# Kernel tuning notes

Measured on AMD Instinct MI355X. Metric: run time of the kernel, lower is better.

The kernel has to match this reference:

```python
import jax, jax.numpy as jnp
import numpy as np

N_NODES = 100000
N_EDGES = 1600000
IN_C = 128
HID = 128
OUT_C = 16
BN_EPS = 1e-5


def _uniform(key, shape, fan_in):
    lim = 1.0 / np.sqrt(fan_in)
    return jax.random.uniform(key, shape, jnp.float32, -lim, lim)


def setup_inputs() -> dict:
    key = jax.random.key(0)
    ks = jax.random.split(key, 24)
    inp = {
        "x": jax.random.normal(ks[0], (N_NODES, IN_C), jnp.float32),
        "edge_index": jax.random.randint(ks[1], (2, N_EDGES), 0, N_NODES, dtype=jnp.int32),
    }
    dims = [(IN_C, HID), (HID, HID), (HID, OUT_C)]
    for l, (fi, fo) in enumerate(dims):
        inp[f"Wn{l}"] = _uniform(ks[2 + 3 * l], (fi, fo), fi)   # lin_l (neighbor) weight
        inp[f"b{l}"] = _uniform(ks[3 + 3 * l], (fo,), fi)        # lin_l bias
        inp[f"Ws{l}"] = _uniform(ks[4 + 3 * l], (fi, fo), fi)   # lin_r (self/root) weight, no bias
    for l in range(2):  # BatchNorm params for the first num_layers-1 layers (eval mode)
        inp[f"g{l}"] = jnp.ones((HID,), jnp.float32)
        inp[f"be{l}"] = jnp.zeros((HID,), jnp.float32)
        inp[f"rm{l}"] = jax.random.normal(ks[12 + 2 * l], (HID,), jnp.float32) * 0.1
        inp[f"rv{l}"] = jax.random.uniform(ks[13 + 2 * l], (HID,), jnp.float32, 0.5, 1.5)
    return inp


def _sage_conv(h, src, dst, Wn, b, Ws):
    # PyG SAGEConv (aggr='mean'): out = lin_l(mean_{j in N(i)} x_j) + lin_r(x_i)
    n = h.shape[0]
    msg = h[src]                                                   # [E, F] gather
    s = jax.ops.segment_sum(msg, dst, num_segments=n)              # [N, F]
    cnt = jax.ops.segment_sum(jnp.ones((src.shape[0], 1), h.dtype), dst, num_segments=n)
    agg = s / jnp.maximum(cnt, 1.0)                                # mean over neighbors
    return agg @ Wn + b + h @ Ws


def _bn_eval(h, g, be, rm, rv):
    return (h - rm) * jax.lax.rsqrt(rv + BN_EPS) * g + be


def reference(x, edge_index, Wn0, b0, Ws0, Wn1, b1, Ws1, Wn2, b2, Ws2,
              g0, be0, rm0, rv0, g1, be1, rm1, rv1):
    src, dst = edge_index[0], edge_index[1]
    h = _sage_conv(x, src, dst, Wn0, b0, Ws0)
    h = jax.nn.relu(_bn_eval(h, g0, be0, rm0, rv0))   # eval: dropout is identity
    h = _sage_conv(h, src, dst, Wn1, b1, Ws1)
    h = jax.nn.relu(_bn_eval(h, g1, be1, rm1, rv1))
    return _sage_conv(h, src, dst, Wn2, b2, Ws2)
```

## Files before the change

kernel.cpp:

```cpp
#include <hip/hip_runtime.h>
#include <hip/hip_bf16.h>


constexpr int N   = 100000;
constexpr int E   = 1600000;
constexpr int F   = 128;
constexpr int FO  = 16;
constexpr int CAP = 64;

typedef __attribute__((ext_vector_type(8))) short bf16x8;
typedef __attribute__((ext_vector_type(4))) float f32x4;

__device__ __forceinline__ ushort f2bf(float v) {
  return __bfloat16_as_ushort(__float2bfloat16(v));
}
__device__ __forceinline__ float bf2f(ushort u) {
  return __uint_as_float(((unsigned)u) << 16);
}
__device__ __forceinline__ float bf_lo(unsigned u) {
  return __uint_as_float(u << 16);
}
__device__ __forceinline__ float bf_hi(unsigned u) {
  return __uint_as_float(u & 0xffff0000u);
}

__global__ void fill_k(const int* __restrict__ src, const int* __restrict__ dst,
                       int* __restrict__ degc, int* __restrict__ slots) {
  int i = blockIdx.x * blockDim.x + threadIdx.x;
  int stride = gridDim.x * blockDim.x;
  for (; i < E; i += stride) {
    int d = dst[i];
    int pos = atomicAdd(&degc[d], 1);
    if (pos < CAP) slots[(size_t)d * CAP + pos] = src[i];
  }
}

__global__ void pack_bt_k(const float* __restrict__ Wn, const float* __restrict__ Ws,
                          ushort* __restrict__ Bt) {
  int t = blockIdx.x * blockDim.x + threadIdx.x;
  int n = t >> 7;
  int k = t & 127;
  float w = (n < 128) ? Wn[k * F + n] : Ws[k * F + (n - 128)];
  Bt[t] = f2bf(w);
}

__global__ __launch_bounds__(256) void dual_gemm_mfma_k(
    const float* __restrict__ h_in, const ushort* __restrict__ Bt,
    const float* __restrict__ b,
    ushort* __restrict__ y, float* __restrict__ s) {
  __shared__ uint4 AsU[2048];
  char* Ahi = reinterpret_cast<char*>(AsU);
  char* Alo = Ahi + 64 * 256;
  const int tid = threadIdx.x;
  const int row0 = blockIdx.x * 64;

#pragma unroll
  for (int j = 0; j < 4; ++j) {
    int f = tid + j * 256;
    int row = f >> 4;
    int kc = f & 15;
    int gr = row0 + row; if (gr >= N) gr = N - 1;
    const float4* gp = reinterpret_cast<const float4*>(h_in + (size_t)gr * F + kc * 8);
    float4 v0 = gp[0], v1 = gp[1];
    float vv[8] = {v0.x, v0.y, v0.z, v0.w, v1.x, v1.y, v1.z, v1.w};
    unsigned ph[4], pl[4];
#pragma unroll
    for (int q = 0; q < 4; ++q) {
      ushort h0 = f2bf(vv[2 * q]);
      ushort h1 = f2bf(vv[2 * q + 1]);
      ushort l0 = f2bf(vv[2 * q] - bf2f(h0));
      ushort l1 = f2bf(vv[2 * q + 1] - bf2f(h1));
      ph[q] = (unsigned)h0 | ((unsigned)h1 << 16);
      pl[q] = (unsigned)l0 | ((unsigned)l1 << 16);
    }
    int off = (row * 256 + kc * 16) ^ ((row & 7) << 4);
    *reinterpret_cast<uint4*>(Ahi + off) = make_uint4(ph[0], ph[1], ph[2], ph[3]);
    *reinterpret_cast<uint4*>(Alo + off) = make_uint4(pl[0], pl[1], pl[2], pl[3]);
  }
  __syncthreads();

  const int lane = tid & 63;
  const int wave = tid >> 6;
  const int wcol0 = wave * 64;
  const int lg = lane >> 4;
  const int lr = lane & 15;

  f32x4 acc[4][4];
#pragma unroll
  for (int r = 0; r < 4; ++r)
#pragma unroll
    for (int c = 0; c < 4; ++c) acc[r][c] = f32x4{0.f, 0.f, 0.f, 0.f};

#pragma unroll
  for (int kk = 0; kk < 4; ++kk) {
    bf16x8 bfr[4];
#pragma unroll
    for (int c = 0; c < 4; ++c) {
      int col = wcol0 + c * 16 + lr;
      bfr[c] = *reinterpret_cast<const bf16x8*>(Bt + (size_t)col * F + kk * 32 + lg * 8);
    }
#pragma unroll
    for (int r = 0; r < 4; ++r) {
      int row = r * 16 + lr;
      int off = (row * 256 + kk * 64 + lg * 16) ^ ((row & 7) << 4);
      bf16x8 a = *reinterpret_cast<const bf16x8*>(Ahi + off);
#pragma unroll
      for (int c = 0; c < 4; ++c)
        acc[r][c] = __builtin_amdgcn_mfma_f32_16x16x32_bf16(a, bfr[c], acc[r][c], 0, 0, 0);
    }
#pragma unroll
    for (int r = 0; r < 4; ++r) {
      int row = r * 16 + lr;
      int off = (row * 256 + kk * 64 + lg * 16) ^ ((row & 7) << 4);
      bf16x8 a = *reinterpret_cast<const bf16x8*>(Alo + off);
#pragma unroll
      for (int c = 0; c < 4; ++c)
        acc[r][c] = __builtin_amdgcn_mfma_f32_16x16x32_bf16(a, bfr[c], acc[r][c], 0, 0, 0);
    }
  }

  if (wave < 2) {
#pragma unroll
    for (int r = 0; r < 4; ++r)
#pragma unroll
      for (int c = 0; c < 4; ++c) {
        int col = wcol0 + c * 16 + lr;
#pragma unroll
        for (int q = 0; q < 4; ++q) {
          int grow = row0 + r * 16 + lg * 4 + q;
          if (grow < N) y[(size_t)grow * F + col] = f2bf(acc[r][c][q]);
        }
      }
  } else {
#pragma unroll
    for (int r = 0; r < 4; ++r)
#pragma unroll
      for (int c = 0; c < 4; ++c) {
        int scol = wcol0 - 128 + c * 16 + lr;
        float bias = b[scol];
#pragma unroll
        for (int q = 0; q < 4; ++q) {
          int grow = row0 + r * 16 + lg * 4 + q;
          if (grow < N) s[(size_t)grow * F + scol] = acc[r][c][q] + bias;
        }
      }
  }
}

__global__ __launch_bounds__(256) void agg_epi_k(
    const int* __restrict__ degc, const int* __restrict__ slots,
    const ushort* __restrict__ y, const float* __restrict__ s,
    const float* __restrict__ g, const float* __restrict__ be,
    const float* __restrict__ rm, const float* __restrict__ rv,
    float* __restrict__ h_out) {
  const int node = blockIdx.x * 4 + (threadIdx.x >> 6);
  const int c2 = threadIdx.x & 63;
  int deg = degc[node]; if (deg > CAP) deg = CAP;
  const int* sl = slots + (size_t)node * CAP;

  float a0 = 0.f, a1 = 0.f, a2 = 0.f, a3 = 0.f;
  float b0 = 0.f, b1 = 0.f, b2 = 0.f, b3 = 0.f;
  int e = 0;
  for (; e + 4 <= deg; e += 4) {
    int n0 = sl[e], n1 = sl[e + 1], n2 = sl[e + 2], n3 = sl[e + 3];
    unsigned u0 = *reinterpret_cast<const unsigned*>(y + (size_t)n0 * F + c2 * 2);
    unsigned u1 = *reinterpret_cast<const unsigned*>(y + (size_t)n1 * F + c2 * 2);
    unsigned u2 = *reinterpret_cast<const unsigned*>(y + (size_t)n2 * F + c2 * 2);
    unsigned u3 = *reinterpret_cast<const unsigned*>(y + (size_t)n3 * F + c2 * 2);
    a0 += bf_lo(u0); b0 += bf_hi(u0);
    a1 += bf_lo(u1); b1 += bf_hi(u1);
    a2 += bf_lo(u2); b2 += bf_hi(u2);
    a3 += bf_lo(u3); b3 += bf_hi(u3);
  }
  for (; e < deg; ++e) {
    unsigned u = *reinterpret_cast<const unsigned*>(y + (size_t)sl[e] * F + c2 * 2);
    a0 += bf_lo(u); b0 += bf_hi(u);
  }
  const float inv = 1.0f / fmaxf((float)deg, 1.0f);
  const float mlo = ((a0 + a1) + (a2 + a3)) * inv;
  const float mhi = ((b0 + b1) + (b2 + b3)) * inv;

  const int cA = 2 * c2;
  float2 sv = *reinterpret_cast<const float2*>(s + (size_t)node * F + cA);
  float2 gv = *reinterpret_cast<const float2*>(g + cA);
  float2 bev = *reinterpret_cast<const float2*>(be + cA);
  float2 rmv = *reinterpret_cast<const float2*>(rm + cA);
  float2 rvv = *reinterpret_cast<const float2*>(rv + cA);
  float olo = (mlo + sv.x - rmv.x) * (rsqrtf(rvv.x + 1e-5f) * gv.x) + bev.x;
  float ohi = (mhi + sv.y - rmv.y) * (rsqrtf(rvv.y + 1e-5f) * gv.y) + bev.y;
  float2 o = make_float2(fmaxf(olo, 0.f), fmaxf(ohi, 0.f));
  *reinterpret_cast<float2*>(h_out + (size_t)node * F + cA) = o;
}

__global__ __launch_bounds__(256) void gemm2_k(
    const float* __restrict__ h_in,
    const float* __restrict__ Wn, const float* __restrict__ Ws,
    const float* __restrict__ b,
    ushort* __restrict__ y2, float* __restrict__ s2) {
  __shared__ float hL[16][F];
  const int tid = threadIdx.x;
  const int row0 = blockIdx.x * 16;
#pragma unroll
  for (int j = 0; j < 2; ++j) {
    int f = tid + j * 256;
    int r = f >> 5;
    int cc = f & 31;
    reinterpret_cast<float4*>(&hL[r][0])[cc] =
        reinterpret_cast<const float4*>(h_in + (size_t)(row0 + r) * F)[cc];
  }
  __syncthreads();

  const int c = tid & 15;
  const int r = tid >> 4;
  float ay = 0.f, as = 0.f;
  for (int k0 = 0; k0 < F; k0 += 4) {
    float4 hv = *reinterpret_cast<const float4*>(&hL[r][k0]);
    ay += hv.x * Wn[(k0 + 0) * FO + c] + hv.y * Wn[(k0 + 1) * FO + c]
        + hv.z * Wn[(k0 + 2) * FO + c] + hv.w * Wn[(k0 + 3) * FO + c];
    as += hv.x * Ws[(k0 + 0) * FO + c] + hv.y * Ws[(k0 + 1) * FO + c]
        + hv.z * Ws[(k0 + 2) * FO + c] + hv.w * Ws[(k0 + 3) * FO + c];
  }
  y2[(size_t)(row0 + r) * FO + c] = f2bf(ay);
  s2[(size_t)(row0 + r) * FO + c] = as + b[c];
}

__global__ __launch_bounds__(256) void agg_out_k(
    const int* __restrict__ degc, const int* __restrict__ slots,
    const ushort* __restrict__ y2, const float* __restrict__ s2,
    float* __restrict__ out) {
  const int node = blockIdx.x * 4 + (threadIdx.x >> 6);
  const int lane = threadIdx.x & 63;
  const int c = lane & 15;
  const int j = lane >> 4;
  int deg = degc[node]; if (deg > CAP) deg = CAP;
  const int* sl = slots + (size_t)node * CAP;
  float acc = 0.f;
  for (int e = j; e < deg; e += 4) {
    unsigned bits = y2[(size_t)sl[e] * FO + c];
    acc += __uint_as_float(bits << 16);
  }
  acc += __shfl_xor(acc, 16, 64);
  acc += __shfl_xor(acc, 32, 64);
  if (j == 0)
    out[(size_t)node * FO + c] = acc / fmaxf((float)deg, 1.0f) + s2[(size_t)node * FO + c];
}

extern "C" void kernel_launch(void* const* d_in, const int* in_sizes, int n_in,
                              void* d_out, int out_size, void* d_ws, size_t ws_size,
                              hipStream_t stream) {
  const float* x   = (const float*)d_in[0];
  const int*   ei  = (const int*)d_in[1];
  const float* Wn0 = (const float*)d_in[2];
  const float* b0  = (const float*)d_in[3];
  const float* Ws0 = (const float*)d_in[4];
  const float* Wn1 = (const float*)d_in[5];
  const float* b1  = (const float*)d_in[6];
  const float* Ws1 = (const float*)d_in[7];
  const float* Wn2 = (const float*)d_in[8];
  const float* b2  = (const float*)d_in[9];
  const float* Ws2 = (const float*)d_in[10];
  const float* g0  = (const float*)d_in[11];
  const float* be0 = (const float*)d_in[12];
  const float* rm0 = (const float*)d_in[13];
  const float* rv0 = (const float*)d_in[14];
  const float* g1  = (const float*)d_in[15];
  const float* be1 = (const float*)d_in[16];
  const float* rm1 = (const float*)d_in[17];
  const float* rv1 = (const float*)d_in[18];

  const int* src = ei;
  const int* dst = ei + E;

  int* degc    = (int*)d_ws;
  int* slots   = degc + N;
  ushort* y    = (ushort*)(slots + (size_t)N * CAP);
  float* s     = (float*)(y + (size_t)N * F);
  float* h     = s + (size_t)N * F;
  ushort* Bt0  = (ushort*)(h + (size_t)N * F);
  ushort* Bt1  = Bt0 + 256 * 128;
  ushort* y2   = y;
  float* s2    = s;

  hipMemsetAsync(degc, 0, N * sizeof(int), stream);
  fill_k<<<2048, 256, 0, stream>>>(src, dst, degc, slots);
  pack_bt_k<<<128, 256, 0, stream>>>(Wn0, Ws0, Bt0);
  pack_bt_k<<<128, 256, 0, stream>>>(Wn1, Ws1, Bt1);

  const int gemm_grid = (N + 63) / 64;

  dual_gemm_mfma_k<<<gemm_grid, 256, 0, stream>>>(x, Bt0, b0, y, s);
  agg_epi_k<<<N / 4, 256, 0, stream>>>(degc, slots, y, s, g0, be0, rm0, rv0, h);

  dual_gemm_mfma_k<<<gemm_grid, 256, 0, stream>>>(h, Bt1, b1, y, s);
  agg_epi_k<<<N / 4, 256, 0, stream>>>(degc, slots, y, s, g1, be1, rm1, rv1, h);

  gemm2_k<<<N / 16, 256, 0, stream>>>(h, Wn2, Ws2, b2, y2, s2);
  agg_out_k<<<N / 4, 256, 0, stream>>>(degc, slots, y2, s2, (float*)d_out);
}
```

Measured before the change: 539.3 us.

## Fuse adjacency fill with first-layer GEMM into one interleaved launch

Merges the edge bucketing (atomic degree count plus slot fill) into the first dual GEMM kernel. Blocks are interleaved in a 3:2 ratio so the memory- and atomic-bound fill runs alongside the MFMA GEMM. The two weight-packing kernels become one launch, and slot writes use nontemporal stores. This removes launches and lets the two independent phases overlap. Fill blocks now reserve the GEMM's shared memory, which may lower occupancy, and the 1042 fill blocks replace the earlier 2048-block grid.

Measured after the change: 510.6 us. 5.3% less time.

```diff
diff --git a/kernel.cpp b/kernel.cpp
--- a/kernel.cpp
+++ b/kernel.cpp
@@ -8,6 +8,10 @@
 constexpr int FO  = 16;
 constexpr int CAP = 64;
 
+constexpr int GEMM_BLOCKS = (N + 63) / 64;
+constexpr int FILL_BLOCKS = 1042;
+constexpr int FUSED_GRID  = GEMM_BLOCKS + FILL_BLOCKS;
+
 typedef __attribute__((ext_vector_type(8))) short bf16x8;
 typedef __attribute__((ext_vector_type(4))) float f32x4;
 
@@ -24,35 +28,28 @@
   return __uint_as_float(u & 0xffff0000u);
 }
 
-__global__ void fill_k(const int* __restrict__ src, const int* __restrict__ dst,
-                       int* __restrict__ degc, int* __restrict__ slots) {
-  int i = blockIdx.x * blockDim.x + threadIdx.x;
-  int stride = gridDim.x * blockDim.x;
-  for (; i < E; i += stride) {
-    int d = dst[i];
-    int pos = atomicAdd(&degc[d], 1);
-    if (pos < CAP) slots[(size_t)d * CAP + pos] = src[i];
-  }
-}
-
-__global__ void pack_bt_k(const float* __restrict__ Wn, const float* __restrict__ Ws,
-                          ushort* __restrict__ Bt) {
+__global__ void pack2_k(const float* __restrict__ Wn0, const float* __restrict__ Ws0,
+                        const float* __restrict__ Wn1, const float* __restrict__ Ws1,
+                        ushort* __restrict__ Bt0, ushort* __restrict__ Bt1) {
   int t = blockIdx.x * blockDim.x + threadIdx.x;
-  int n = t >> 7;
-  int k = t & 127;
+  int which = t >> 15;
+  int i = t & 32767;
+  int n = i >> 7;
+  int k = i & 127;
+  const float* Wn = which ? Wn1 : Wn0;
+  const float* Ws = which ? Ws1 : Ws0;
+  ushort* Bt = which ? Bt1 : Bt0;
   float w = (n < 128) ? Wn[k * F + n] : Ws[k * F + (n - 128)];
-  Bt[t] = f2bf(w);
-}
-
-__global__ __launch_bounds__(256) void dual_gemm_mfma_k(
+  Bt[i] = f2bf(w);
+}
+
+__device__ __forceinline__ void gemm_body(
+    int bg, int tid,
     const float* __restrict__ h_in, const ushort* __restrict__ Bt,
     const float* __restrict__ b,
-    ushort* __restrict__ y, float* __restrict__ s) {
-  __shared__ uint4 AsU[2048];
-  char* Ahi = reinterpret_cast<char*>(AsU);
-  char* Alo = Ahi + 64 * 256;
-  const int tid = threadIdx.x;
-  const int row0 = blockIdx.x * 64;
+    ushort* __restrict__ y, float* __restrict__ s,
+    char* Ahi, char* Alo) {
+  const int row0 = bg * 64;
 
 #pragma unroll
   for (int j = 0; j < 4; ++j) {
@@ -145,6 +142,44 @@
         }
       }
   }
+}
+
+__global__ __launch_bounds__(256) void fused0_k(
+    const float* __restrict__ x, const ushort* __restrict__ Bt0,
+    const float* __restrict__ b0,
+    ushort* __restrict__ y, float* __restrict__ s,
+    const int* __restrict__ src, const int* __restrict__ dst,
+    int* __restrict__ degc, int* __restrict__ slots) {
+  __shared__ uint4 AsU[2048];
+  char* Ahi = reinterpret_cast<char*>(AsU);
+  char* Alo = Ahi + 64 * 256;
+  const int gid = blockIdx.x;
+  const int grp = gid / 5, rem = gid % 5;
+  const int tid = threadIdx.x;
+
+  if (rem < 3) {
+    gemm_body(grp * 3 + rem, tid, x, Bt0, b0, y, s, Ahi, Alo);
+  } else {
+    const int bf = grp * 2 + (rem - 3);
+    int i = bf * 256 + tid;
+    const int stride = FILL_BLOCKS * 256;
+    for (; i < E; i += stride) {
+      int d = dst[i];
+      int pos = atomicAdd(&degc[d], 1);
+      if (pos < CAP)
+        __builtin_nontemporal_store(src[i], &slots[(size_t)d * CAP + pos]);
+    }
+  }
+}
+
+__global__ __launch_bounds__(256) void dual_gemm_mfma_k(
+    const float* __restrict__ h_in, const ushort* __restrict__ Bt,
+    const float* __restrict__ b,
+    ushort* __restrict__ y, float* __restrict__ s) {
+  __shared__ uint4 AsU[2048];
+  char* Ahi = reinterpret_cast<char*>(AsU);
+  char* Alo = Ahi + 64 * 256;
+  gemm_body(blockIdx.x, threadIdx.x, h_in, Bt, b, y, s, Ahi, Alo);
 }
 
 __global__ __launch_bounds__(256) void agg_epi_k(
@@ -282,16 +317,12 @@
   float* s2    = s;
 
   hipMemsetAsync(degc, 0, N * sizeof(int), stream);
-  fill_k<<<2048, 256, 0, stream>>>(src, dst, degc, slots);
-  pack_bt_k<<<128, 256, 0, stream>>>(Wn0, Ws0, Bt0);
-  pack_bt_k<<<128, 256, 0, stream>>>(Wn1, Ws1, Bt1);
-
-  const int gemm_grid = (N + 63) / 64;
-
-  dual_gemm_mfma_k<<<gemm_grid, 256, 0, stream>>>(x, Bt0, b0, y, s);
+  pack2_k<<<256, 256, 0, stream>>>(Wn0, Ws0, Wn1, Ws1, Bt0, Bt1);
+
+  fused0_k<<<FUSED_GRID, 256, 0, stream>>>(x, Bt0, b0, y, s, src, dst, degc, slots);
   agg_epi_k<<<N / 4, 256, 0, stream>>>(degc, slots, y, s, g0, be0, rm0, rv0, h);
 
-  dual_gemm_mfma_k<<<gemm_grid, 256, 0, stream>>>(h, Bt1, b1, y, s);
+  dual_gemm_mfma_k<<<GEMM_BLOCKS, 256, 0, stream>>>(h, Bt1, b1, y, s);
   agg_epi_k<<<N / 4, 256, 0, stream>>>(degc, slots, y, s, g1, be1, rm1, rv1, h);
 
   gemm2_k<<<N / 16, 256, 0, stream>>>(h, Wn2, Ws2, b2, y2, s2);
```
